# Performance work log

Measured on AMD Instinct MI355X. Metric: run time of the kernel, lower is better.

## Reference

```python
import jax, jax.numpy as jnp
import numpy as np

NUM_HEADS = 12
HEAD_SIZE = 64
B1, B2 = 28, 52          # get_block_sizes(use_dynamic=False): (1456//52, 52)
NUM_FRAMES = 2
SEQ = NUM_FRAMES * B1 * B2   # 2912
BATCH = 1
SCALE = HEAD_SIZE ** -0.5


def _rope(x, cos, sin):
    # interleaved rotary (is_neox_style=False); x [B,T,H,D], cos/sin [T,D//2]
    x1, x2 = x[..., 0::2], x[..., 1::2]
    c, s = cos[:, None, :], sin[:, None, :]
    o1 = x1 * c - x2 * s
    o2 = x2 * c + x1 * s
    return jnp.stack([o1, o2], axis=-1).reshape(x.shape)


def _blin(x, W, b):
    # per-head (batched replicated) linear: x [..., H, Din], W [H, Dout, Din], b [H, Dout]
    return jnp.einsum('...hd,hed->...he', x, W) + b


def _sdpa(q, k, v):
    # q [N,1,H,D], k/v [N,L,H,D] -> [N,1,H,D]
    s = jnp.einsum('nqhd,nkhd->nhqk', q, k) * SCALE
    p = jax.nn.softmax(s, axis=-1)
    return jnp.einsum('nhqk,nkhd->nqhd', p, v)


def _forward(lq, lk, rq, rk, v, cos, sin,
             W_lkq, b_lkq, W_lkk, b_lkk, W_lkv, b_lkv,
             W_rqq, b_rqq, W_rqk, b_rqk, W_rqv, b_rqv):
    B, S, H, D = lq.shape
    F = S // (B1 * B2)
    hd2 = D // 2
    lq_r = _rope(lq, cos, sin).reshape(B, F, B1, B2, H, D)
    # ---- left factor: local attention over b2 within each (frame, b1) block ----
    lkq = lk.reshape(B, F, B1, B2, H, D)[:, :, :, 0]           # [B,F,B1,H,D]
    lkq = _blin(lkq, W_lkq, b_lkq)
    cos_k = cos.reshape(F, B1, B2, hd2)[:, :, 0].reshape(F * B1, hd2)
    sin_k = sin.reshape(F, B1, B2, hd2)[:, :, 0].reshape(F * B1, hd2)
    lkq = _rope(lkq.reshape(B, F * B1, H, D), cos_k, sin_k).reshape(B, F, B1, H, D)
    lkk = _rope(_blin(lk, W_lkk, b_lkk), cos, sin).reshape(B, F, B1, B2, H, D)
    lkv = _blin(lk, W_lkv, b_lkv).reshape(B, F, B1, B2, H, D)
    x = _sdpa(lkq.reshape(-1, 1, H, D), lkk.reshape(-1, B2, H, D), lkv.reshape(-1, B2, H, D))
    lk_out = _rope(x.reshape(B, F * B1, H, D), cos_k, sin_k).reshape(B, F, B1, H, D)
    L = jnp.einsum('baijhd,bfkhd->bhafjik', lq_r, lk_out)      # [B,H,F,F,B2,B1,B1]
    # ---- right factor: local attention over b1 for each (frame, b2) slice ----
    rk_r = _rope(rk, cos, sin).reshape(B, F, B1, B2, H, D)
    rqq = rq.reshape(B, F, B1, B2, H, D)[:, :, 0]              # [B,F,B2,H,D]
    rqq = _blin(rqq, W_rqq, b_rqq)
    cos_j = cos.reshape(F, B1, B2, hd2)[:, 0].reshape(F * B2, hd2)
    sin_j = sin.reshape(F, B1, B2, hd2)[:, 0].reshape(F * B2, hd2)
    rqq = _rope(rqq.reshape(B, F * B2, H, D), cos_j, sin_j).reshape(B, F, B2, H, D)
    rqk = _rope(_blin(rq, W_rqk, b_rqk), cos, sin).reshape(B, F, B1, B2, H, D)
    rqv = _blin(rq, W_rqv, b_rqv).reshape(B, F, B1, B2, H, D)
    kq = jnp.transpose(rqk, (0, 1, 3, 2, 4, 5)).reshape(-1, B1, H, D)  # (b f j) i h d
    vq = jnp.transpose(rqv, (0, 1, 3, 2, 4, 5)).reshape(-1, B1, H, D)
    x = _sdpa(rqq.reshape(-1, 1, H, D), kq, vq)
    rq_out = _rope(x.reshape(B, F * B2, H, D), cos_j, sin_j).reshape(B, F, B2, H, D)
    R = jnp.einsum('bajhd,bfklhd->bhafkjl', rq_out, rk_r)      # [B,H,F,F,B1,B2,B2]
    # ---- combine factors into full logits, softmax, apply to v ----
    out = jnp.einsum('bhafjik,bhafkjl->bhafijkl', L, R)        # [B,H,F,F,B1,B2,B1,B2]
    out = jnp.transpose(out, (0, 1, 2, 4, 5, 3, 6, 7)).reshape(B, H, S, S)
    p = jax.nn.softmax(out * SCALE, axis=-1)
    return jnp.einsum('bhsl,blhd->bshd', p, v)


def setup_inputs() -> dict:
    key = jax.random.key(0)
    ks = jax.random.split(key, 20)
    shp = (BATCH, SEQ, NUM_HEADS, HEAD_SIZE)
    f = lambda k, s: jax.random.normal(k, s, dtype=jnp.float32)
    inp = {'lq': f(ks[0], shp), 'lk': f(ks[1], shp), 'rq': f(ks[2], shp),
           'rk': f(ks[3], shp), 'v': f(ks[4], shp)}
    pos = jnp.arange(SEQ, dtype=jnp.float32)
    inv = 1.0 / (10000.0 ** (jnp.arange(0, HEAD_SIZE, 2, dtype=jnp.float32) / HEAD_SIZE))
    ang = pos[:, None] * inv[None, :]
    inp['cos'], inp['sin'] = jnp.cos(ang), jnp.sin(ang)
    for i, n in enumerate(['lkq', 'lkk', 'lkv', 'rqq', 'rqk', 'rqv']):
        inp['W_' + n] = f(ks[5 + 2 * i], (NUM_HEADS, HEAD_SIZE, HEAD_SIZE)) * (HEAD_SIZE ** -0.5)
        inp['b_' + n] = f(ks[6 + 2 * i], (NUM_HEADS, HEAD_SIZE)) * 0.02
    return inp


def reference(lq, lk, rq, rk, v, cos, sin,
              W_lkq, b_lkq, W_lkk, b_lkk, W_lkv, b_lkv,
              W_rqq, b_rqq, W_rqk, b_rqk, W_rqv, b_rqv):
    return _forward(lq, lk, rq, rk, v, cos, sin,
                    W_lkq, b_lkq, W_lkk, b_lkk, W_lkv, b_lkv,
                    W_rqq, b_rqq, W_rqk, b_rqk, W_rqv, b_rqv)
```

## Files before the change

### kernel.cpp

```cpp
#include <hip/hip_runtime.h>
#include <hip/hip_bf16.h>

#define HH 12
#define DD 64
#define NB1 28
#define NB2 52
#define NF 2
#define FB1 56
#define FB2 104
#define STRIDE_HD 768
#define SCALEF 0.125f

typedef float f32x4 __attribute__((ext_vector_type(4)));
typedef float f32x16 __attribute__((ext_vector_type(16)));
typedef short bf16x8 __attribute__((ext_vector_type(8)));

#if __has_builtin(__builtin_amdgcn_exp2f)
#define EXP2(x) __builtin_amdgcn_exp2f(x)
#else
#define EXP2(x) __expf((x) * 0.6931471805599453f)
#endif

__device__ __forceinline__ unsigned short f2bf(float x) {
  union { float f; unsigned u; } c; c.f = x;
  unsigned r = c.u + 0x7fffu + ((c.u >> 16) & 1u);
  return (unsigned short)(r >> 16);
}

__global__ __launch_bounds__(256, 4)
void k_proj(const float* __restrict__ lk, const float* __restrict__ rq,
            const float* __restrict__ cosb, const float* __restrict__ sinb,
            const float* __restrict__ W_lkk, const float* __restrict__ b_lkk,
            const float* __restrict__ W_rqk, const float* __restrict__ b_rqk,
            const float* __restrict__ W_lkq, const float* __restrict__ b_lkq,
            const float* __restrict__ W_rqq, const float* __restrict__ b_rqq,
            float* __restrict__ Klg, float* __restrict__ Krg,
            float* __restrict__ ql, float* __restrict__ qr) {
  __shared__ __align__(16) float Wt[64][68];
  __shared__ __align__(16) float xs[64][68];
  __shared__ int srows[64];
  __shared__ int obase[64];

  const int tid = threadIdx.x;
  int bx = blockIdx.x;
  int path, h, c;
  if (bx < 552)       { path = 0; h = bx / 46; c = bx % 46; }
  else if (bx < 1104) { path = 1; bx -= 552;  h = bx / 46; c = bx % 46; }
  else if (bx < 1116) { path = 2; h = bx - 1104; c = 0; }
  else                { path = 3; bx -= 1116; h = bx >> 1; c = bx & 1; }

  const float* X  = (path == 1 || path == 3) ? rq : lk;
  const float* W  = (path == 0) ? W_lkk : (path == 1) ? W_rqk : (path == 2) ? W_lkq : W_rqq;
  const float* bb = (path == 0) ? b_lkk : (path == 1) ? b_rqk : (path == 2) ? b_lkq : b_rqq;
  float* out      = (path == 0) ? Klg : (path == 1) ? Krg : (path == 2) ? ql : qr;
  const int nrows = (path == 0 || path == 1) ? ((c == 45) ? 32 : 64)
                   : (path == 2) ? 56 : ((c == 1) ? 40 : 64);

  for (int idx = tid; idx < 4096; idx += 256)
    Wt[idx & 63][idx >> 6] = W[(size_t)h * 4096 + idx];
  if (tid < 64) {
    int rr = tid, s = 0, ob = 0;
    if (rr < nrows) {
      if (path == 0) {
        s = c * 64 + rr;
        int f = s / 1456, rem = s % 1456, b1 = rem / 52, b2 = rem % 52;
        ob = ((h * 56 + f * 28 + b1) * 52 + b2) * 64;
      } else if (path == 1) {
        s = c * 64 + rr;
        int f = s / 1456, rem = s % 1456, b1 = rem / 52, jj = rem % 52;
        ob = ((h * 104 + f * 52 + jj) * 28 + b1) * 64;
      } else if (path == 2) {
        int q = rr;
        s = (q / 28) * 1456 + (q % 28) * 52;
        ob = (h * 56 + q) * 64;
      } else {
        int q = c * 64 + rr;
        s = (q / 52) * 1456 + (q % 52);
        ob = (h * 104 + q) * 64;
      }
    }
    srows[rr] = s; obase[rr] = ob;
  }
  __syncthreads();
  for (int idx = tid; idx < 4096; idx += 256) {
    int r = idx >> 6, d = idx & 63;
    xs[r][d] = X[(size_t)srows[r] * STRIDE_HD + h * DD + d];
  }
  __syncthreads();

  const int it = tid >> 4, kt = tid & 15;
  f32x4 acc0 = {0,0,0,0}, acc1 = {0,0,0,0}, acc2 = {0,0,0,0}, acc3 = {0,0,0,0};
  #pragma unroll 4
  for (int d4 = 0; d4 < 16; ++d4) {
    f32x4 x0 = *(const f32x4*)&xs[4 * it][4 * d4];
    f32x4 x1 = *(const f32x4*)&xs[4 * it + 1][4 * d4];
    f32x4 x2 = *(const f32x4*)&xs[4 * it + 2][4 * d4];
    f32x4 x3 = *(const f32x4*)&xs[4 * it + 3][4 * d4];
    #pragma unroll
    for (int dd = 0; dd < 4; ++dd) {
      f32x4 wv = *(const f32x4*)&Wt[4 * d4 + dd][4 * kt];
      acc0 += x0[dd] * wv;
      acc1 += x1[dd] * wv;
      acc2 += x2[dd] * wv;
      acc3 += x3[dd] * wv;
    }
  }

  f32x4 bv;
  bv[0] = bb[h * 64 + 4 * kt];     bv[1] = bb[h * 64 + 4 * kt + 1];
  bv[2] = bb[h * 64 + 4 * kt + 2]; bv[3] = bb[h * 64 + 4 * kt + 3];
  #pragma unroll
  for (int rr = 0; rr < 4; ++rr) {
    int row = 4 * it + rr;
    if (row < nrows) {
      f32x4 o = (rr == 0) ? acc0 : (rr == 1) ? acc1 : (rr == 2) ? acc2 : acc3;
      o += bv;
      int s = srows[row];
      float c0 = cosb[s * 32 + 2 * kt],     s0 = sinb[s * 32 + 2 * kt];
      float c1 = cosb[s * 32 + 2 * kt + 1], s1 = sinb[s * 32 + 2 * kt + 1];
      f32x4 res;
      res[0] = o[0] * c0 - o[1] * s0;
      res[1] = o[1] * c0 + o[0] * s0;
      res[2] = o[2] * c1 - o[3] * s1;
      res[3] = o[3] * c1 + o[2] * s1;
      *(f32x4*)(out + obase[row] + 4 * kt) = res;
    }
  }
}

struct SvShared {
  union {
    struct { float qv[64]; float sc[64]; float ps[64]; float ys[64]; float oe[64]; } s;
    float tile[52][68];
  } u;
};

template<int NK, int NG, int GD, int GMUL, int KSTR>
__device__ void sdpa_path(int n, int h, const float* __restrict__ X,
                          const float* __restrict__ Kg, const float* __restrict__ qb,
                          const float* __restrict__ cosb, const float* __restrict__ sinb,
                          const float* __restrict__ Wv, const float* __restrict__ bvv,
                          float* __restrict__ outb, SvShared& sm) {
  const int t = threadIdx.x;
  const int f = n / GD, g = n % GD;
  const int s_base = f * (NB1 * NB2) + g * GMUL;

  if (t < 64) sm.u.s.qv[t] = qb[(size_t)(h * NG + n) * 64 + t];
  __syncthreads();

  if (t < NK * 4) {
    int r = t >> 2, part = t & 3;
    const float4* kr = (const float4*)(Kg + ((size_t)(h * NG + n) * NK + r) * 64 + part * 16);
    const float4* q4 = (const float4*)(sm.u.s.qv + part * 16);
    float p = 0.f;
    #pragma unroll
    for (int i = 0; i < 4; ++i) {
      float4 kv = kr[i], qv4 = q4[i];
      p += kv.x * qv4.x + kv.y * qv4.y + kv.z * qv4.z + kv.w * qv4.w;
    }
    p += __shfl_xor(p, 1); p += __shfl_xor(p, 2);
    if (part == 0) sm.u.s.sc[r] = p * SCALEF;
  }
  __syncthreads();

  if (t < 64) {
    float v = (t < NK) ? sm.u.s.sc[t] : -1e30f;
    float mx = v;
    for (int o = 32; o; o >>= 1) mx = fmaxf(mx, __shfl_xor(mx, o));
    float e = (t < NK) ? __expf(v - mx) : 0.f;
    float sum = e;
    for (int o = 32; o; o >>= 1) sum += __shfl_xor(sum, o);
    sm.u.s.ps[t] = (t < NK) ? e / sum : 0.f;
  }
  __syncthreads();

  {
    int d = t >> 2, g4 = t & 3;
    constexpr int RPG = NK / 4;
    float yp = 0.f;
    #pragma unroll 4
    for (int rr = 0; rr < RPG; ++rr) {
      int r = g4 * RPG + rr;
      yp += sm.u.s.ps[r] * X[(size_t)(s_base + r * KSTR) * STRIDE_HD + h * DD + d];
    }
    yp += __shfl_xor(yp, 1); yp += __shfl_xor(yp, 2);
    if (g4 == 0) sm.u.s.ys[d] = yp;
  }
  __syncthreads();

  {
    int e = t >> 2, part = t & 3;
    const float4* wr = (const float4*)(Wv + (size_t)h * 4096 + e * 64 + part * 16);
    const float4* y4 = (const float4*)(sm.u.s.ys + part * 16);
    float p = 0.f;
    #pragma unroll
    for (int i = 0; i < 4; ++i) {
      float4 wv = wr[i], yv = y4[i];
      p += wv.x * yv.x + wv.y * yv.y + wv.z * yv.z + wv.w * yv.w;
    }
    p += __shfl_xor(p, 1); p += __shfl_xor(p, 2);
    if (part == 0) sm.u.s.oe[e] = p + bvv[h * 64 + e];
  }
  __syncthreads();

  if (t < 32) {
    float co = cosb[s_base * 32 + t], si = sinb[s_base * 32 + t];
    float o0 = sm.u.s.oe[2 * t], o1 = sm.u.s.oe[2 * t + 1];
    outb[(size_t)n * STRIDE_HD + h * DD + 2 * t]     = o0 * co - o1 * si;
    outb[(size_t)n * STRIDE_HD + h * DD + 2 * t + 1] = o1 * co + o0 * si;
  }
}

__device__ void vb_path(int fk, int h, const float* __restrict__ v,
                        unsigned short* __restrict__ vb2, SvShared& sm) {
  const int tid = threadIdx.x;
  for (int idx = tid; idx < NB2 * DD; idx += 256) {
    int l = idx >> 6, d = idx & 63;
    sm.u.tile[l][d] = v[(size_t)(fk * NB2 + l) * STRIDE_HD + h * DD + d];
  }
  __syncthreads();
  for (int idx = tid; idx < 512; idx += 256) {
    int l8 = idx >> 6, d = idx & 63;
    unsigned short tmp[8];
    #pragma unroll
    for (int li = 0; li < 8; ++li) {
      int l = l8 * 8 + li;
      tmp[li] = (l < NB2) ? f2bf(sm.u.tile[l][d]) : (unsigned short)0;
    }
    bf16x8* dst = (bf16x8*)(vb2 + (((size_t)(h * FB1 + fk) * 8 + l8) * 64 + d) * 8);
    *dst = *(bf16x8*)tmp;
  }
}

__global__ __launch_bounds__(256)
void k_sv(const float* __restrict__ lk, const float* __restrict__ rq,
          const float* __restrict__ v,
          const float* __restrict__ cosb, const float* __restrict__ sinb,
          const float* __restrict__ Klg, const float* __restrict__ Krg,
          const float* __restrict__ ql, const float* __restrict__ qr,
          const float* __restrict__ W_lkv, const float* __restrict__ b_lkv,
          const float* __restrict__ W_rqv, const float* __restrict__ b_rqv,
          float* __restrict__ lk_out, float* __restrict__ rq_out,
          unsigned short* __restrict__ vb2) {
  __shared__ SvShared sm;
  const int bx = blockIdx.x;
  if (bx < 672) {
    sdpa_path<52, 56, 28, 52, 1>(bx % 56, bx / 56, lk, Klg, ql, cosb, sinb,
                                 W_lkv, b_lkv, lk_out, sm);
  } else if (bx < 1920) {
    int id = bx - 672;
    sdpa_path<28, 104, 52, 1, 52>(id % 104, id / 104, rq, Krg, qr, cosb, sinb,
                                  W_rqv, b_rqv, rq_out, sm);
  } else {
    int id = bx - 1920;
    vb_path(id % 56, id / 56, v, vb2, sm);
  }
}

struct MidLShared { float qs[NB1][68]; float ks[FB1][68]; };
struct MidRShared { float ks[NB2][68]; float qs[FB2][68]; };
union MidShared { MidLShared L; MidRShared R; };

__device__ void L_path(int bid, const float* __restrict__ lq,
                       const float* __restrict__ cosb, const float* __restrict__ sinb,
                       const float* __restrict__ lk_out, float* __restrict__ Lbuf,
                       MidLShared& sh) {
  const int h = bid / (NF * NB2);
  const int rem = bid % (NF * NB2);
  const int a = rem / NB2, j = rem % NB2;
  const int tid = threadIdx.x;
  for (int idx = tid; idx < NB1 * 32; idx += 256) {
    int i = idx >> 5, mm = idx & 31;
    int srow = a * (NB1 * NB2) + i * NB2 + j;
    const float* xr = lq + (size_t)srow * STRIDE_HD + h * DD;
    float x0 = xr[2 * mm], x1 = xr[2 * mm + 1];
    float co = cosb[srow * 32 + mm], si = sinb[srow * 32 + mm];
    sh.qs[i][2 * mm]     = x0 * co - x1 * si;
    sh.qs[i][2 * mm + 1] = x1 * co + x0 * si;
  }
  for (int idx = tid; idx < FB1 * DD; idx += 256) {
    int r = idx >> 6, d = idx & 63;
    sh.ks[r][d] = lk_out[(size_t)r * STRIDE_HD + h * DD + d];
  }
  __syncthreads();
  for (int t = tid; t < NF * 14 * 14; t += 256) {
    int ff = t / 196, rr = t % 196;
    int it = rr / 14, kt = rr % 14;
    const float4* q0 = (const float4*)sh.qs[2 * it];
    const float4* q1 = (const float4*)sh.qs[2 * it + 1];
    const float4* k0 = (const float4*)sh.ks[ff * NB1 + 2 * kt];
    const float4* k1 = (const float4*)sh.ks[ff * NB1 + 2 * kt + 1];
    float a00 = 0.f, a01 = 0.f, a10 = 0.f, a11 = 0.f;
    #pragma unroll
    for (int d4 = 0; d4 < 16; ++d4) {
      float4 qa = q0[d4], qb = q1[d4], ka = k0[d4], kb = k1[d4];
      a00 += qa.x * ka.x + qa.y * ka.y + qa.z * ka.z + qa.w * ka.w;
      a01 += qa.x * kb.x + qa.y * kb.y + qa.z * kb.z + qa.w * kb.w;
      a10 += qb.x * ka.x + qb.y * ka.y + qb.z * ka.z + qb.w * ka.w;
      a11 += qb.x * kb.x + qb.y * kb.y + qb.z * kb.z + qb.w * kb.w;
    }
    size_t ob = (size_t)bid * (NF * NB1 * NB1) + (size_t)ff * (NB1 * NB1);
    Lbuf[ob + (size_t)(2 * it) * NB1 + 2 * kt]         = a00;
    Lbuf[ob + (size_t)(2 * it) * NB1 + 2 * kt + 1]     = a01;
    Lbuf[ob + (size_t)(2 * it + 1) * NB1 + 2 * kt]     = a10;
    Lbuf[ob + (size_t)(2 * it + 1) * NB1 + 2 * kt + 1] = a11;
  }
}

__device__ void R_path(int bid, const float* __restrict__ rk,
                       const float* __restrict__ cosb, const float* __restrict__ sinb,
                       const float* __restrict__ rq_out, float* __restrict__ Rbuf,
                       MidRShared& sh) {
  const int h = bid / FB1;
  const int fk = bid % FB1;
  const int f = fk / NB1, k = fk % NB1;
  const int tid = threadIdx.x;
  for (int idx = tid; idx < NB2 * 32; idx += 256) {
    int l = idx >> 5, mm = idx & 31;
    int srow = f * (NB1 * NB2) + k * NB2 + l;
    const float* xr = rk + (size_t)srow * STRIDE_HD + h * DD;
    float x0 = xr[2 * mm], x1 = xr[2 * mm + 1];
    float co = cosb[srow * 32 + mm], si = sinb[srow * 32 + mm];
    sh.ks[l][2 * mm]     = x0 * co - x1 * si;
    sh.ks[l][2 * mm + 1] = x1 * co + x0 * si;
  }
  for (int idx = tid; idx < FB2 * DD; idx += 256) {
    int r2 = idx >> 6, d = idx & 63;
    sh.qs[r2][d] = rq_out[(size_t)r2 * STRIDE_HD + h * DD + d];
  }
  __syncthreads();
  for (int t = tid; t < NF * 26 * 26; t += 256) {
    int aa = t / 676, rr = t % 676;
    int jt = rr / 26, lt = rr % 26;
    const float4* q0 = (const float4*)sh.qs[aa * NB2 + 2 * jt];
    const float4* q1 = (const float4*)sh.qs[aa * NB2 + 2 * jt + 1];
    const float4* k0 = (const float4*)sh.ks[2 * lt];
    const float4* k1 = (const float4*)sh.ks[2 * lt + 1];
    float a00 = 0.f, a01 = 0.f, a10 = 0.f, a11 = 0.f;
    #pragma unroll
    for (int d4 = 0; d4 < 16; ++d4) {
      float4 qa = q0[d4], qb = q1[d4], ka = k0[d4], kb = k1[d4];
      a00 += qa.x * ka.x + qa.y * ka.y + qa.z * ka.z + qa.w * ka.w;
      a01 += qa.x * kb.x + qa.y * kb.y + qa.z * kb.z + qa.w * kb.w;
      a10 += qb.x * ka.x + qb.y * ka.y + qb.z * ka.z + qb.w * ka.w;
      a11 += qb.x * kb.x + qb.y * kb.y + qb.z * kb.z + qb.w * kb.w;
    }
    size_t row0 = ((size_t)(h * NF + aa) * NB2 + 2 * jt) * (size_t)(NF * NB1 * NB2);
    size_t row1 = row0 + (size_t)(NF * NB1 * NB2);
    size_t cb = (size_t)fk * NB2 + 2 * lt;
    Rbuf[row0 + cb]     = a00;
    Rbuf[row0 + cb + 1] = a01;
    Rbuf[row1 + cb]     = a10;
    Rbuf[row1 + cb + 1] = a11;
  }
}

__global__ __launch_bounds__(256)
void k_mid(const float* __restrict__ lq, const float* __restrict__ rk,
           const float* __restrict__ cosb, const float* __restrict__ sinb,
           const float* __restrict__ lk_out, const float* __restrict__ rq_out,
           float* __restrict__ Lbuf, float* __restrict__ Rbuf) {
  __shared__ __align__(16) MidShared sh;
  const int bx = blockIdx.x;
  if (bx < 1248) L_path(bx, lq, cosb, sinb, lk_out, Lbuf, sh.L);
  else           R_path(bx - 1248, rk, cosb, sinb, rq_out, Rbuf, sh.R);
}

struct MainPro { float Ls2T[2][28][36]; float Rs[56][64]; };
union MainShared { MainPro p; float epil[4][16][64]; };

__global__ __launch_bounds__(256, 4)
void k_main(const float* __restrict__ Lbuf, const float* __restrict__ Rbuf,
            const unsigned short* __restrict__ vb2, float* __restrict__ outp) {
  const int bid0 = blockIdx.x;
  const int bid = (bid0 & 7) * 156 + (bid0 >> 3);
  const int h = bid / (NF * NB2);
  const int rem = bid % (NF * NB2);
  const int a = rem / NB2, j = rem % NB2;
  const int tid = threadIdx.x;
  const int lane = tid & 63;
  const int w = tid >> 6;

  __shared__ __align__(16) MainShared ms;
  __shared__ float m2s[32], Rmx[FB1], Rmn[FB1], els[4][32];

  const float SC = SCALEF * 1.44269504f;
  for (int idx = tid; idx < NF * NB1 * NB1; idx += 256) {
    int ff = idx / 784, r2 = idx % 784;
    int i = r2 / 28, kk = r2 % 28;
    ms.p.Ls2T[ff][kk][i] = Lbuf[(size_t)bid * (NF * NB1 * NB1) + idx] * SC;
  }
  if (tid < 224) {
    int ff = tid / 112, r2 = tid % 112;
    ms.p.Ls2T[ff][r2 >> 2][28 + (r2 & 3)] = 0.f;
  }
  for (int idx = tid; idx < FB1 * 13; idx += 256) {
    int fk = idx / 13, lc = idx % 13;
    float4 vv = ((const float4*)(Rbuf + (size_t)bid * (NF * NB1 * NB2)))[idx];
    *(float4*)&ms.p.Rs[fk][lc * 4] = vv;
  }
  if (tid >= 252) m2s[tid - 224] = 0.f;
  __syncthreads();

  if (tid < 224) {
    int fk = tid >> 2, part = tid & 3;
    float mx = -1e30f, mn = 1e30f;
    for (int l = part * 13; l < part * 13 + 13; ++l) {
      float x = ms.p.Rs[fk][l];
      mx = fmaxf(mx, x); mn = fminf(mn, x);
    }
    mx = fmaxf(mx, __shfl_xor(mx, 1)); mn = fminf(mn, __shfl_xor(mn, 1));
    mx = fmaxf(mx, __shfl_xor(mx, 2)); mn = fminf(mn, __shfl_xor(mn, 2));
    if (part == 0) { Rmx[fk] = mx; Rmn[fk] = mn; }
  }
  __syncthreads();

  if (tid < 224) {
    int i = tid >> 3, s = tid & 7;
    float m = -1e30f;
    #pragma unroll
    for (int n = 0; n < 7; ++n) {
      int fk = s + 8 * n;
      int ff = (fk >= NB1) ? 1 : 0, kk = fk - ff * NB1;
      float Lv = ms.p.Ls2T[ff][kk][i];
      m = fmaxf(m, fmaxf(Lv * Rmx[fk], Lv * Rmn[fk]));
    }
    m = fmaxf(m, __shfl_xor(m, 1));
    m = fmaxf(m, __shfl_xor(m, 2));
    m = fmaxf(m, __shfl_xor(m, 4));
    if (s == 0) m2s[i] = m;
  }
  __syncthreads();

  const int row = lane & 31;
  const int hi = lane >> 5;
  const float nm = -m2s[row];
  const bf16x8* vw = (const bf16x8*)vb2 + (size_t)h * 28672 + hi * 64 + row;

  f32x16 acc0 = {0.f,0.f,0.f,0.f,0.f,0.f,0.f,0.f,0.f,0.f,0.f,0.f,0.f,0.f,0.f,0.f};
  f32x16 acc1 = {0.f,0.f,0.f,0.f,0.f,0.f,0.f,0.f,0.f,0.f,0.f,0.f,0.f,0.f,0.f,0.f};
  float lsum = 0.f;

  for (int t = 0; t < 14; ++t) {
    const int fk = w * 14 + t;
    const float Lv = ms.p.Ls2T[w >> 1][(w & 1) * 14 + t][row];
    const bf16x8* vp = vw + (size_t)fk * 512;
    #pragma unroll
    for (int ks = 0; ks < 4; ++ks) {
      const int k0 = ks * 16 + hi * 8;
      float4 ra = *(const float4*)&ms.p.Rs[fk][k0];
      float4 rb = *(const float4*)&ms.p.Rs[fk][k0 + 4];
      float p0 = EXP2(fmaf(Lv, ra.x, nm));
      float p1 = EXP2(fmaf(Lv, ra.y, nm));
      float p2 = EXP2(fmaf(Lv, ra.z, nm));
      float p3 = EXP2(fmaf(Lv, ra.w, nm));
      float p4 = EXP2(fmaf(Lv, rb.x, nm));
      float p5 = EXP2(fmaf(Lv, rb.y, nm));
      float p6 = EXP2(fmaf(Lv, rb.z, nm));
      float p7 = EXP2(fmaf(Lv, rb.w, nm));
      if (ks == 3) {
        if (hi == 0) { p4 = 0.f; p5 = 0.f; p6 = 0.f; p7 = 0.f; }
        else { p0 = 0.f; p1 = 0.f; p2 = 0.f; p3 = 0.f;
               p4 = 0.f; p5 = 0.f; p6 = 0.f; p7 = 0.f; }
      }
      lsum += ((p0 + p1) + (p2 + p3)) + ((p4 + p5) + (p6 + p7));
      union { bf16x8 v8; __hip_bfloat162 h2[4]; } pk;
      pk.h2[0] = __float22bfloat162_rn(make_float2(p0, p1));
      pk.h2[1] = __float22bfloat162_rn(make_float2(p2, p3));
      pk.h2[2] = __float22bfloat162_rn(make_float2(p4, p5));
      pk.h2[3] = __float22bfloat162_rn(make_float2(p6, p7));
      bf16x8 b0 = vp[ks * 128];
      bf16x8 b1 = vp[ks * 128 + 32];
      acc0 = __builtin_amdgcn_mfma_f32_32x32x16_bf16(pk.v8, b0, acc0, 0, 0, 0);
      acc1 = __builtin_amdgcn_mfma_f32_32x32x16_bf16(pk.v8, b1, acc1, 0, 0, 0);
    }
  }

  lsum += __shfl_xor(lsum, 32);
  if (lane < 32) els[w][lane] = lsum;
  __syncthreads();

  #pragma unroll
  for (int half = 0; half < 2; ++half) {
    if (half) __syncthreads();
    #pragma unroll
    for (int r = 0; r < 16; ++r)
      ms.epil[w][r][lane] = half ? acc1[r] : acc0[r];
    __syncthreads();
    #pragma unroll
    for (int q = 0; q < 4; ++q) {
      int r = (tid >> 6) + q * 4;
      int elane = tid & 63;
      float val = ms.epil[0][r][elane] + ms.epil[1][r][elane]
                + ms.epil[2][r][elane] + ms.epil[3][r][elane];
      int irow = (r & 3) + 8 * (r >> 2) + 4 * (elane >> 5);
      if (irow < NB1) {
        float li = 1.0f / (els[0][irow] + els[1][irow] + els[2][irow] + els[3][irow]);
        int srow = a * (NB1 * NB2) + irow * NB2 + j;
        int d = half * 32 + (elane & 31);
        outp[(size_t)srow * STRIDE_HD + h * DD + d] = val * li;
      }
    }
  }
}

extern "C" void kernel_launch(void* const* d_in, const int* in_sizes, int n_in,
                              void* d_out, int out_size, void* d_ws, size_t ws_size,
                              hipStream_t stream) {
  (void)in_sizes; (void)n_in; (void)out_size; (void)ws_size;
  const float* lq   = (const float*)d_in[0];
  const float* lk   = (const float*)d_in[1];
  const float* rq   = (const float*)d_in[2];
  const float* rk   = (const float*)d_in[3];
  const float* v    = (const float*)d_in[4];
  const float* cosb = (const float*)d_in[5];
  const float* sinb = (const float*)d_in[6];
  const float* W_lkq = (const float*)d_in[7];  const float* b_lkq = (const float*)d_in[8];
  const float* W_lkk = (const float*)d_in[9];  const float* b_lkk = (const float*)d_in[10];
  const float* W_lkv = (const float*)d_in[11]; const float* b_lkv = (const float*)d_in[12];
  const float* W_rqq = (const float*)d_in[13]; const float* b_rqq = (const float*)d_in[14];
  const float* W_rqk = (const float*)d_in[15]; const float* b_rqk = (const float*)d_in[16];
  const float* W_rqv = (const float*)d_in[17]; const float* b_rqv = (const float*)d_in[18];

  float* ws = (float*)d_ws;
  float* lk_out = ws;
  float* rq_out = ws + 43008;
  float* Lbuf   = ws + 122880;
  float* Rbuf   = ws + 2079744;
  unsigned short* vb2 = (unsigned short*)(ws + 5713920);
  float* ql     = ws + 7090176;
  float* qr     = ws + 7133184;
  float* Klg = Lbuf;
  float* Krg = Lbuf + 2236416;

  k_proj<<<1140, 256, 0, stream>>>(lk, rq, cosb, sinb,
      W_lkk, b_lkk, W_rqk, b_rqk, W_lkq, b_lkq, W_rqq, b_rqq,
      Klg, Krg, ql, qr);
  k_sv<<<2592, 256, 0, stream>>>(lk, rq, v, cosb, sinb, Klg, Krg, ql, qr,
      W_lkv, b_lkv, W_rqv, b_rqv, lk_out, rq_out, vb2);
  k_mid<<<1920, 256, 0, stream>>>(lq, rk, cosb, sinb, lk_out, rq_out, Lbuf, Rbuf);
  k_main<<<1248, 256, 0, stream>>>(Lbuf, Rbuf, vb2, (float*)d_out);
}
```

Measured before the change: 111.4 us.

## Use 4x4 register tiles in k_mid and split R path by frame

The L and R dot-product loops in k_mid now give each thread a 4x4 output tile instead of 2x2, so each value loaded from shared memory feeds more FMAs. The results are written with float4 global stores. The R path is split into two blocks per (h,fk), one per query frame, which halves its shared q buffer and raises the grid from 1920 to 2592 blocks. Launch bounds now request 4 blocks per SM. In exchange, only 98 of 256 threads (L) or 169 of 256 (R) do the compute phase, and the rk rope load is repeated in both R blocks.

```diff
diff --git a/kernel.cpp b/kernel.cpp
--- a/kernel.cpp
+++ b/kernel.cpp
@@ -258,7 +258,7 @@
 }
 
 struct MidLShared { float qs[NB1][68]; float ks[FB1][68]; };
-struct MidRShared { float ks[NB2][68]; float qs[FB2][68]; };
+struct MidRShared { float ks[NB2][68]; float qs[NB2][68]; };
 union MidShared { MidLShared L; MidRShared R; };
 
 __device__ void L_path(int bid, const float* __restrict__ lq,
@@ -283,27 +283,40 @@
     sh.ks[r][d] = lk_out[(size_t)r * STRIDE_HD + h * DD + d];
   }
   __syncthreads();
-  for (int t = tid; t < NF * 14 * 14; t += 256) {
-    int ff = t / 196, rr = t % 196;
-    int it = rr / 14, kt = rr % 14;
-    const float4* q0 = (const float4*)sh.qs[2 * it];
-    const float4* q1 = (const float4*)sh.qs[2 * it + 1];
-    const float4* k0 = (const float4*)sh.ks[ff * NB1 + 2 * kt];
-    const float4* k1 = (const float4*)sh.ks[ff * NB1 + 2 * kt + 1];
-    float a00 = 0.f, a01 = 0.f, a10 = 0.f, a11 = 0.f;
-    #pragma unroll
+  if (tid < NF * 49) {
+    int ff = tid / 49, rr2 = tid % 49;
+    int it = rr2 / 7, kt = rr2 % 7;
+    float acc[4][4] = {{0,0,0,0},{0,0,0,0},{0,0,0,0},{0,0,0,0}};
+    #pragma unroll 4
     for (int d4 = 0; d4 < 16; ++d4) {
-      float4 qa = q0[d4], qb = q1[d4], ka = k0[d4], kb = k1[d4];
-      a00 += qa.x * ka.x + qa.y * ka.y + qa.z * ka.z + qa.w * ka.w;
-      a01 += qa.x * kb.x + qa.y * kb.y + qa.z * kb.z + qa.w * kb.w;
-      a10 += qb.x * ka.x + qb.y * ka.y + qb.z * ka.z + qb.w * ka.w;
-      a11 += qb.x * kb.x + qb.y * kb.y + qb.z * kb.z + qb.w * kb.w;
+      f32x4 q0 = *(const f32x4*)&sh.qs[4 * it][4 * d4];
+      f32x4 q1 = *(const f32x4*)&sh.qs[4 * it + 1][4 * d4];
+      f32x4 q2 = *(const f32x4*)&sh.qs[4 * it + 2][4 * d4];
+      f32x4 q3 = *(const f32x4*)&sh.qs[4 * it + 3][4 * d4];
+      f32x4 k0 = *(const f32x4*)&sh.ks[ff * NB1 + 4 * kt][4 * d4];
+      f32x4 k1 = *(const f32x4*)&sh.ks[ff * NB1 + 4 * kt + 1][4 * d4];
+      f32x4 k2 = *(const f32x4*)&sh.ks[ff * NB1 + 4 * kt + 2][4 * d4];
+      f32x4 k3 = *(const f32x4*)&sh.ks[ff * NB1 + 4 * kt + 3][4 * d4];
+      #pragma unroll
+      for (int dd = 0; dd < 4; ++dd) {
+        float qv0 = q0[dd], qv1 = q1[dd], qv2 = q2[dd], qv3 = q3[dd];
+        float kv0 = k0[dd], kv1 = k1[dd], kv2 = k2[dd], kv3 = k3[dd];
+        acc[0][0] += qv0 * kv0; acc[0][1] += qv0 * kv1;
+        acc[0][2] += qv0 * kv2; acc[0][3] += qv0 * kv3;
+        acc[1][0] += qv1 * kv0; acc[1][1] += qv1 * kv1;
+        acc[1][2] += qv1 * kv2; acc[1][3] += qv1 * kv3;
+        acc[2][0] += qv2 * kv0; acc[2][1] += qv2 * kv1;
+        acc[2][2] += qv2 * kv2; acc[2][3] += qv2 * kv3;
+        acc[3][0] += qv3 * kv0; acc[3][1] += qv3 * kv1;
+        acc[3][2] += qv3 * kv2; acc[3][3] += qv3 * kv3;
+      }
     }
     size_t ob = (size_t)bid * (NF * NB1 * NB1) + (size_t)ff * (NB1 * NB1);
-    Lbuf[ob + (size_t)(2 * it) * NB1 + 2 * kt]         = a00;
-    Lbuf[ob + (size_t)(2 * it) * NB1 + 2 * kt + 1]     = a01;
-    Lbuf[ob + (size_t)(2 * it + 1) * NB1 + 2 * kt]     = a10;
-    Lbuf[ob + (size_t)(2 * it + 1) * NB1 + 2 * kt + 1] = a11;
+    #pragma unroll
+    for (int r = 0; r < 4; ++r) {
+      f32x4 res = {acc[r][0], acc[r][1], acc[r][2], acc[r][3]};
+      *(f32x4*)&Lbuf[ob + (size_t)(4 * it + r) * NB1 + 4 * kt] = res;
+    }
   }
 }
 
@@ -311,8 +324,9 @@
                        const float* __restrict__ cosb, const float* __restrict__ sinb,
                        const float* __restrict__ rq_out, float* __restrict__ Rbuf,
                        MidRShared& sh) {
-  const int h = bid / FB1;
-  const int fk = bid % FB1;
+  const int h = bid / 112;
+  const int rem = bid % 112;
+  const int fk = rem >> 1, aa = rem & 1;
   const int f = fk / NB1, k = fk % NB1;
   const int tid = threadIdx.x;
   for (int idx = tid; idx < NB2 * 32; idx += 256) {
@@ -324,38 +338,49 @@
     sh.ks[l][2 * mm]     = x0 * co - x1 * si;
     sh.ks[l][2 * mm + 1] = x1 * co + x0 * si;
   }
-  for (int idx = tid; idx < FB2 * DD; idx += 256) {
+  for (int idx = tid; idx < NB2 * DD; idx += 256) {
     int r2 = idx >> 6, d = idx & 63;
-    sh.qs[r2][d] = rq_out[(size_t)r2 * STRIDE_HD + h * DD + d];
-  }
-  __syncthreads();
-  for (int t = tid; t < NF * 26 * 26; t += 256) {
-    int aa = t / 676, rr = t % 676;
-    int jt = rr / 26, lt = rr % 26;
-    const float4* q0 = (const float4*)sh.qs[aa * NB2 + 2 * jt];
-    const float4* q1 = (const float4*)sh.qs[aa * NB2 + 2 * jt + 1];
-    const float4* k0 = (const float4*)sh.ks[2 * lt];
-    const float4* k1 = (const float4*)sh.ks[2 * lt + 1];
-    float a00 = 0.f, a01 = 0.f, a10 = 0.f, a11 = 0.f;
-    #pragma unroll
+    sh.qs[r2][d] = rq_out[(size_t)(aa * NB2 + r2) * STRIDE_HD + h * DD + d];
+  }
+  __syncthreads();
+  if (tid < 169) {
+    int jt = tid / 13, lt = tid % 13;
+    float acc[4][4] = {{0,0,0,0},{0,0,0,0},{0,0,0,0},{0,0,0,0}};
+    #pragma unroll 4
     for (int d4 = 0; d4 < 16; ++d4) {
-      float4 qa = q0[d4], qb = q1[d4], ka = k0[d4], kb = k1[d4];
-      a00 += qa.x * ka.x + qa.y * ka.y + qa.z * ka.z + qa.w * ka.w;
-      a01 += qa.x * kb.x + qa.y * kb.y + qa.z * kb.z + qa.w * kb.w;
-      a10 += qb.x * ka.x + qb.y * ka.y + qb.z * ka.z + qb.w * ka.w;
-      a11 += qb.x * kb.x + qb.y * kb.y + qb.z * kb.z + qb.w * kb.w;
-    }
-    size_t row0 = ((size_t)(h * NF + aa) * NB2 + 2 * jt) * (size_t)(NF * NB1 * NB2);
-    size_t row1 = row0 + (size_t)(NF * NB1 * NB2);
-    size_t cb = (size_t)fk * NB2 + 2 * lt;
-    Rbuf[row0 + cb]     = a00;
-    Rbuf[row0 + cb + 1] = a01;
-    Rbuf[row1 + cb]     = a10;
-    Rbuf[row1 + cb + 1] = a11;
-  }
-}
-
-__global__ __launch_bounds__(256)
+      f32x4 q0 = *(const f32x4*)&sh.qs[4 * jt][4 * d4];
+      f32x4 q1 = *(const f32x4*)&sh.qs[4 * jt + 1][4 * d4];
+      f32x4 q2 = *(const f32x4*)&sh.qs[4 * jt + 2][4 * d4];
+      f32x4 q3 = *(const f32x4*)&sh.qs[4 * jt + 3][4 * d4];
+      f32x4 k0 = *(const f32x4*)&sh.ks[4 * lt][4 * d4];
+      f32x4 k1 = *(const f32x4*)&sh.ks[4 * lt + 1][4 * d4];
+      f32x4 k2 = *(const f32x4*)&sh.ks[4 * lt + 2][4 * d4];
+      f32x4 k3 = *(const f32x4*)&sh.ks[4 * lt + 3][4 * d4];
+      #pragma unroll
+      for (int dd = 0; dd < 4; ++dd) {
+        float qv0 = q0[dd], qv1 = q1[dd], qv2 = q2[dd], qv3 = q3[dd];
+        float kv0 = k0[dd], kv1 = k1[dd], kv2 = k2[dd], kv3 = k3[dd];
+        acc[0][0] += qv0 * kv0; acc[0][1] += qv0 * kv1;
+        acc[0][2] += qv0 * kv2; acc[0][3] += qv0 * kv3;
+        acc[1][0] += qv1 * kv0; acc[1][1] += qv1 * kv1;
+        acc[1][2] += qv1 * kv2; acc[1][3] += qv1 * kv3;
+        acc[2][0] += qv2 * kv0; acc[2][1] += qv2 * kv1;
+        acc[2][2] += qv2 * kv2; acc[2][3] += qv2 * kv3;
+        acc[3][0] += qv3 * kv0; acc[3][1] += qv3 * kv1;
+        acc[3][2] += qv3 * kv2; acc[3][3] += qv3 * kv3;
+      }
+    }
+    #pragma unroll
+    for (int r = 0; r < 4; ++r) {
+      size_t rowb = ((size_t)(h * NF + aa) * NB2 + 4 * jt + r) * (size_t)(NF * NB1 * NB2)
+                  + (size_t)fk * NB2 + 4 * lt;
+      f32x4 res = {acc[r][0], acc[r][1], acc[r][2], acc[r][3]};
+      *(f32x4*)&Rbuf[rowb] = res;
+    }
+  }
+}
+
+__global__ __launch_bounds__(256, 4)
 void k_mid(const float* __restrict__ lq, const float* __restrict__ rk,
            const float* __restrict__ cosb, const float* __restrict__ sinb,
            const float* __restrict__ lk_out, const float* __restrict__ rq_out,
@@ -538,6 +563,6 @@
       Klg, Krg, ql, qr);
   k_sv<<<2592, 256, 0, stream>>>(lk, rq, v, cosb, sinb, Klg, Krg, ql, qr,
       W_lkv, b_lkv, W_rqv, b_rqv, lk_out, rq_out, vb2);
-  k_mid<<<1920, 256, 0, stream>>>(lq, rk, cosb, sinb, lk_out, rq_out, Lbuf, Rbuf);
+  k_mid<<<2592, 256, 0, stream>>>(lq, rk, cosb, sinb, lk_out, rq_out, Lbuf, Rbuf);
   k_main<<<1248, 256, 0, stream>>>(Lbuf, Rbuf, vb2, (float*)d_out);
 }
```

After: 111.8 us. Within noise of the previous version (+0.4%).

## Compute mid-stage L/R factor products with split-bf16 MFMA GEMM kernels

Applied to the files above, without the earlier changes.

Replaces the scalar FP32 L/R dot-product mid kernel with a templated kernel that treats each factor as a GEMM over all sequence rows per head. Operands are split into bf16 hi/lo parts (three MFMA passes approximating fp32), stored in swizzled LDS, with the small K-side operand held in registers. The grid drops from 1920 blocks to two 156-block launches, each block looping over 7 row tiles. This aims to cut redundant operand loading and use matrix cores, at the cost of fewer blocks (lower occupancy) and slight precision loss from the 3-term bf16 split.

```diff
diff --git a/kernel.cpp b/kernel.cpp
--- a/kernel.cpp
+++ b/kernel.cpp
@@ -25,6 +25,9 @@
   union { float f; unsigned u; } c; c.f = x;
   unsigned r = c.u + 0x7fffu + ((c.u >> 16) & 1u);
   return (unsigned short)(r >> 16);
+}
+__device__ __forceinline__ float bf2f(unsigned short u) {
+  union { unsigned u32v; float f; } c; c.u32v = ((unsigned)u) << 16; return c.f;
 }
 
 __global__ __launch_bounds__(256, 4)
@@ -257,113 +260,111 @@
   }
 }
 
-struct MidLShared { float qs[NB1][68]; float ks[FB1][68]; };
-struct MidRShared { float ks[NB2][68]; float qs[FB2][68]; };
-union MidShared { MidLShared L; MidRShared R; };
-
-__device__ void L_path(int bid, const float* __restrict__ lq,
-                       const float* __restrict__ cosb, const float* __restrict__ sinb,
-                       const float* __restrict__ lk_out, float* __restrict__ Lbuf,
-                       MidLShared& sh) {
-  const int h = bid / (NF * NB2);
-  const int rem = bid % (NF * NB2);
-  const int a = rem / NB2, j = rem % NB2;
+template<int QROWS, int QV, int NTHR, int PATH>
+__global__ __launch_bounds__(NTHR)
+void k_midg(const float* __restrict__ X, const float* __restrict__ Yb,
+            const float* __restrict__ cosb, const float* __restrict__ sinb,
+            float* __restrict__ outb) {
+  const int bx = blockIdx.x;
+  const int h = bx / 13, chunk = bx % 13;
   const int tid = threadIdx.x;
-  for (int idx = tid; idx < NB1 * 32; idx += 256) {
-    int i = idx >> 5, mm = idx & 31;
-    int srow = a * (NB1 * NB2) + i * NB2 + j;
-    const float* xr = lq + (size_t)srow * STRIDE_HD + h * DD;
-    float x0 = xr[2 * mm], x1 = xr[2 * mm + 1];
-    float co = cosb[srow * 32 + mm], si = sinb[srow * 32 + mm];
-    sh.qs[i][2 * mm]     = x0 * co - x1 * si;
-    sh.qs[i][2 * mm + 1] = x1 * co + x0 * si;
-  }
-  for (int idx = tid; idx < FB1 * DD; idx += 256) {
-    int r = idx >> 6, d = idx & 63;
-    sh.ks[r][d] = lk_out[(size_t)r * STRIDE_HD + h * DD + d];
-  }
-  __syncthreads();
-  for (int t = tid; t < NF * 14 * 14; t += 256) {
-    int ff = t / 196, rr = t % 196;
-    int it = rr / 14, kt = rr % 14;
-    const float4* q0 = (const float4*)sh.qs[2 * it];
-    const float4* q1 = (const float4*)sh.qs[2 * it + 1];
-    const float4* k0 = (const float4*)sh.ks[ff * NB1 + 2 * kt];
-    const float4* k1 = (const float4*)sh.ks[ff * NB1 + 2 * kt + 1];
-    float a00 = 0.f, a01 = 0.f, a10 = 0.f, a11 = 0.f;
-    #pragma unroll
-    for (int d4 = 0; d4 < 16; ++d4) {
-      float4 qa = q0[d4], qb = q1[d4], ka = k0[d4], kb = k1[d4];
-      a00 += qa.x * ka.x + qa.y * ka.y + qa.z * ka.z + qa.w * ka.w;
-      a01 += qa.x * kb.x + qa.y * kb.y + qa.z * kb.z + qa.w * kb.w;
-      a10 += qb.x * ka.x + qb.y * ka.y + qb.z * ka.z + qb.w * ka.w;
-      a11 += qb.x * kb.x + qb.y * kb.y + qb.z * kb.z + qb.w * kb.w;
-    }
-    size_t ob = (size_t)bid * (NF * NB1 * NB1) + (size_t)ff * (NB1 * NB1);
-    Lbuf[ob + (size_t)(2 * it) * NB1 + 2 * kt]         = a00;
-    Lbuf[ob + (size_t)(2 * it) * NB1 + 2 * kt + 1]     = a01;
-    Lbuf[ob + (size_t)(2 * it + 1) * NB1 + 2 * kt]     = a10;
-    Lbuf[ob + (size_t)(2 * it + 1) * NB1 + 2 * kt + 1] = a11;
-  }
-}
-
-__device__ void R_path(int bid, const float* __restrict__ rk,
-                       const float* __restrict__ cosb, const float* __restrict__ sinb,
-                       const float* __restrict__ rq_out, float* __restrict__ Rbuf,
-                       MidRShared& sh) {
-  const int h = bid / FB1;
-  const int fk = bid % FB1;
-  const int f = fk / NB1, k = fk % NB1;
-  const int tid = threadIdx.x;
-  for (int idx = tid; idx < NB2 * 32; idx += 256) {
-    int l = idx >> 5, mm = idx & 31;
-    int srow = f * (NB1 * NB2) + k * NB2 + l;
-    const float* xr = rk + (size_t)srow * STRIDE_HD + h * DD;
-    float x0 = xr[2 * mm], x1 = xr[2 * mm + 1];
-    float co = cosb[srow * 32 + mm], si = sinb[srow * 32 + mm];
-    sh.ks[l][2 * mm]     = x0 * co - x1 * si;
-    sh.ks[l][2 * mm + 1] = x1 * co + x0 * si;
-  }
-  for (int idx = tid; idx < FB2 * DD; idx += 256) {
-    int r2 = idx >> 6, d = idx & 63;
-    sh.qs[r2][d] = rq_out[(size_t)r2 * STRIDE_HD + h * DD + d];
-  }
-  __syncthreads();
-  for (int t = tid; t < NF * 26 * 26; t += 256) {
-    int aa = t / 676, rr = t % 676;
-    int jt = rr / 26, lt = rr % 26;
-    const float4* q0 = (const float4*)sh.qs[aa * NB2 + 2 * jt];
-    const float4* q1 = (const float4*)sh.qs[aa * NB2 + 2 * jt + 1];
-    const float4* k0 = (const float4*)sh.ks[2 * lt];
-    const float4* k1 = (const float4*)sh.ks[2 * lt + 1];
-    float a00 = 0.f, a01 = 0.f, a10 = 0.f, a11 = 0.f;
-    #pragma unroll
-    for (int d4 = 0; d4 < 16; ++d4) {
-      float4 qa = q0[d4], qb = q1[d4], ka = k0[d4], kb = k1[d4];
-      a00 += qa.x * ka.x + qa.y * ka.y + qa.z * ka.z + qa.w * ka.w;
-      a01 += qa.x * kb.x + qa.y * kb.y + qa.z * kb.z + qa.w * kb.w;
-      a10 += qb.x * ka.x + qb.y * ka.y + qb.z * ka.z + qb.w * ka.w;
-      a11 += qb.x * kb.x + qb.y * kb.y + qb.z * kb.z + qb.w * kb.w;
-    }
-    size_t row0 = ((size_t)(h * NF + aa) * NB2 + 2 * jt) * (size_t)(NF * NB1 * NB2);
-    size_t row1 = row0 + (size_t)(NF * NB1 * NB2);
-    size_t cb = (size_t)fk * NB2 + 2 * lt;
-    Rbuf[row0 + cb]     = a00;
-    Rbuf[row0 + cb + 1] = a01;
-    Rbuf[row1 + cb]     = a10;
-    Rbuf[row1 + cb + 1] = a11;
-  }
-}
-
-__global__ __launch_bounds__(256)
-void k_mid(const float* __restrict__ lq, const float* __restrict__ rk,
-           const float* __restrict__ cosb, const float* __restrict__ sinb,
-           const float* __restrict__ lk_out, const float* __restrict__ rq_out,
-           float* __restrict__ Lbuf, float* __restrict__ Rbuf) {
-  __shared__ __align__(16) MidShared sh;
-  const int bx = blockIdx.x;
-  if (bx < 1248) L_path(bx, lq, cosb, sinb, lk_out, Lbuf, sh.L);
-  else           R_path(bx - 1248, rk, cosb, sinb, rq_out, Rbuf, sh.R);
+  const int lane = tid & 63;
+  const int qt = tid >> 6;
+  const int hi = lane >> 5;
+  const int arow = lane & 31;
+
+  __shared__ __align__(16) unsigned short Yhi[QROWS][64];
+  __shared__ __align__(16) unsigned short Ylo[QROWS][64];
+  __shared__ __align__(16) unsigned short Xhi[32][64];
+  __shared__ __align__(16) unsigned short Xlo[32][64];
+
+  for (int idx = tid; idx < QROWS * 32; idx += NTHR) {
+    int q = idx >> 5, m = idx & 31;
+    float y0 = 0.f, y1 = 0.f;
+    if (q < QV) {
+      float2 yv = *(const float2*)(Yb + (size_t)q * STRIDE_HD + h * DD + 2 * m);
+      y0 = yv.x; y1 = yv.y;
+    }
+    unsigned short h0 = f2bf(y0), h1 = f2bf(y1);
+    unsigned short l0 = f2bf(y0 - bf2f(h0)), l1 = f2bf(y1 - bf2f(h1));
+    int ms = m ^ ((q & 7) << 2);
+    ((unsigned*)Yhi[q])[ms] = (unsigned)h0 | ((unsigned)h1 << 16);
+    ((unsigned*)Ylo[q])[ms] = (unsigned)l0 | ((unsigned)l1 << 16);
+  }
+  __syncthreads();
+
+  bf16x8 Bhi[4], Blo[4];
+  {
+    const int brow = qt * 32 + arow;
+    const int bswz = (brow & 7) << 3;
+    #pragma unroll
+    for (int ks = 0; ks < 4; ++ks) {
+      int kb = (ks * 16 + hi * 8) ^ bswz;
+      Bhi[ks] = *(const bf16x8*)&Yhi[brow][kb];
+      Blo[ks] = *(const bf16x8*)&Ylo[brow][kb];
+    }
+  }
+
+  for (int t = 0; t < 7; ++t) {
+    const int rowbase = (chunk * 7 + t) * 32;
+    for (int pidx = tid; pidx < 1024; pidx += NTHR) {
+      int r = pidx >> 5, m = pidx & 31;
+      int srow = rowbase + r;
+      float2 xv = *(const float2*)(X + (size_t)srow * STRIDE_HD + h * DD + 2 * m);
+      float co = cosb[srow * 32 + m], si = sinb[srow * 32 + m];
+      float o0 = xv.x * co - xv.y * si;
+      float o1 = xv.y * co + xv.x * si;
+      unsigned short h0 = f2bf(o0), h1 = f2bf(o1);
+      unsigned short l0 = f2bf(o0 - bf2f(h0)), l1 = f2bf(o1 - bf2f(h1));
+      int ms = m ^ ((r & 7) << 2);
+      ((unsigned*)Xhi[r])[ms] = (unsigned)h0 | ((unsigned)h1 << 16);
+      ((unsigned*)Xlo[r])[ms] = (unsigned)l0 | ((unsigned)l1 << 16);
+    }
+    __syncthreads();
+
+    f32x16 acc = {0.f,0.f,0.f,0.f,0.f,0.f,0.f,0.f,0.f,0.f,0.f,0.f,0.f,0.f,0.f,0.f};
+    {
+      const int aswz = (arow & 7) << 3;
+      #pragma unroll
+      for (int ks = 0; ks < 4; ++ks) {
+        int kb = (ks * 16 + hi * 8) ^ aswz;
+        bf16x8 Ahi = *(const bf16x8*)&Xhi[arow][kb];
+        bf16x8 Alo = *(const bf16x8*)&Xlo[arow][kb];
+        acc = __builtin_amdgcn_mfma_f32_32x32x16_bf16(Ahi, Bhi[ks], acc, 0, 0, 0);
+        acc = __builtin_amdgcn_mfma_f32_32x32x16_bf16(Ahi, Blo[ks], acc, 0, 0, 0);
+        acc = __builtin_amdgcn_mfma_f32_32x32x16_bf16(Alo, Bhi[ks], acc, 0, 0, 0);
+      }
+    }
+
+    if (PATH == 0) {
+      int col = qt * 32 + arow;
+      if (col < 56) {
+        int f = (col >= 28) ? 1 : 0;
+        int k = col - f * 28;
+        #pragma unroll
+        for (int rg = 0; rg < 16; ++rg) {
+          int P = rowbase + (rg & 3) + 8 * (rg >> 2) + 4 * hi;
+          int a = (P >= 1456) ? 1 : 0;
+          int rem2 = P - a * 1456;
+          int i = rem2 / 52, j = rem2 - i * 52;
+          outb[((size_t)(h * 104 + a * 52 + j)) * 1568 + f * 784 + i * 28 + k] = acc[rg];
+        }
+      }
+    } else {
+      int cq = qt * 32 + arow;
+      if (cq < 104) {
+        int aa = (cq >= 52) ? 1 : 0;
+        int jj = cq - aa * 52;
+        float* rowp = outb + ((size_t)((h * 2 + aa) * 52 + jj)) * 2912 + rowbase + 4 * hi;
+        #pragma unroll
+        for (int q4 = 0; q4 < 4; ++q4) {
+          f32x4 res = {acc[4 * q4], acc[4 * q4 + 1], acc[4 * q4 + 2], acc[4 * q4 + 3]};
+          *(f32x4*)(rowp + 8 * q4) = res;
+        }
+      }
+    }
+    __syncthreads();
+  }
 }
 
 struct MainPro { float Ls2T[2][28][36]; float Rs[56][64]; };
@@ -538,6 +539,7 @@
       Klg, Krg, ql, qr);
   k_sv<<<2592, 256, 0, stream>>>(lk, rq, v, cosb, sinb, Klg, Krg, ql, qr,
       W_lkv, b_lkv, W_rqv, b_rqv, lk_out, rq_out, vb2);
-  k_mid<<<1920, 256, 0, stream>>>(lq, rk, cosb, sinb, lk_out, rq_out, Lbuf, Rbuf);
+  k_midg<64, 56, 128, 0><<<156, 128, 0, stream>>>(lq, lk_out, cosb, sinb, Lbuf);
+  k_midg<128, 104, 256, 1><<<156, 256, 0, stream>>>(rk, rq_out, cosb, sinb, Rbuf);
   k_main<<<1248, 256, 0, stream>>>(Lbuf, Rbuf, vb2, (float*)d_out);
 }
```

Result: slower. 131.8 us (+18.4%).
